# Kernel tuning notes

Measured on AMD Instinct MI355X. Metric: run time of the kernel, lower is better.

Reference implementation:

```python
import jax, jax.numpy as jnp
import numpy as np

NOISE_EPS = 1e-2   # Shazeer noisy-gating stddev floor
LN_EPS = 1e-6
LOSS_COEF = 0.01
K = 2              # num_activated_experts


def _layer_norm(x, w, b):
    mu = jnp.mean(x, axis=-1, keepdims=True)
    var = jnp.var(x, axis=-1, keepdims=True)
    return (x - mu) * jax.lax.rsqrt(var + LN_EPS) * w + b


def _cv_squared(v):
    return jnp.var(v) / (jnp.mean(v) ** 2 + 1e-10)


def _normal_cdf(z):
    return 0.5 * (1.0 + jax.scipy.special.erf(z / jnp.sqrt(jnp.asarray(2.0, z.dtype))))


def setup_inputs() -> dict:
    key = jax.random.key(0)
    ks = jax.random.split(key, 8)
    N, D, H, O, E = 8192, 512, 1024, 512, 8
    x = jax.random.normal(ks[0], (N, D), jnp.float32)
    x_offsets = jnp.sort(jax.random.randint(ks[1], (17,), 0, N)).astype(jnp.int64)
    noise = jax.random.normal(ks[2], (N, E), jnp.float32)
    s = 0.02
    return {
        "x": x,
        "x_offsets": x_offsets,
        "max_seq_len": 2048,
        "noise": noise,
        "norm_w": jnp.ones((D,), jnp.float32),
        "norm_bias": jnp.zeros((D,), jnp.float32),
        "w_gate": jax.random.normal(ks[3], (D, E), jnp.float32) * s,
        "w_noise": jax.random.normal(ks[4], (D, E), jnp.float32) * s,
        "W1": jax.random.normal(ks[5], (E, H, D), jnp.float32) * s,  # [E, model_d, input]
        "b1": jnp.zeros((E, H), jnp.float32),
        "W2": jax.random.normal(ks[6], (E, O, H), jnp.float32) * s,  # [E, output, model_d]
        "b2": jnp.zeros((E, O), jnp.float32),
        "output_weight": jax.random.normal(ks[7], (D, O), jnp.float32) * s,
    }


def reference(x, x_offsets, max_seq_len, noise, norm_w, norm_bias, w_gate, w_noise,
              W1, b1, W2, b2, output_weight):
    N, D = x.shape
    E = w_gate.shape[1]
    k_plus = min(K + 1, E)

    # pre-norm
    x_norm = _layer_norm(x, norm_w, norm_bias)

    # noisy top-k gating (training path)
    clean_logits = x_norm @ w_gate                      # [N, E]
    noise_stddev = jax.nn.softplus(x_norm @ w_noise) + NOISE_EPS
    noisy_logits = clean_logits + noise * noise_stddev

    top_logits, top_indices = jax.lax.top_k(noisy_logits, k_plus)   # [N, k+1]
    top_k_logits = top_logits[:, :K]
    top_k_indices = top_indices[:, :K]
    top_k_gates = jax.nn.softmax(top_k_logits, axis=-1)             # [N, K]

    rows = jnp.arange(N)[:, None]
    gates = jnp.zeros((N, E), top_k_gates.dtype).at[rows, top_k_indices].set(top_k_gates)

    # load = prob each expert is in top-k under the gating noise (Shazeer)
    flat = top_logits.reshape(-1)
    pos_in = jnp.arange(N) * k_plus + K
    thr_in = flat[pos_in][:, None]          # (k+1)-th value: threshold if already in
    thr_out = flat[pos_in - 1][:, None]     # k-th value: threshold if currently out
    is_in = noisy_logits > thr_in
    prob_in = _normal_cdf((clean_logits - thr_in) / noise_stddev)
    prob_out = _normal_cdf((clean_logits - thr_out) / noise_stddev)
    load_probs = jnp.where(is_in, prob_in, prob_out)                # [N, E]

    loss = LOSS_COEF * (_cv_squared(gates.sum(0)) + _cv_squared(load_probs.sum(0)))

    # dispatch stats: tokens per expert
    lengths = jnp.zeros((E,), jnp.float32).at[top_k_indices.reshape(-1)].add(1.0)
    load = lengths / lengths.sum()

    # grouped expert MLP (dense one-hot combine; gates are 0 for unrouted experts)
    h = jnp.einsum('nd,ehd->neh', x_norm, W1) + b1                  # [N, E, H]
    a = jax.nn.silu(h)
    y_e = jnp.einsum('neh,eoh->neo', a, W2) + b2                    # [N, E, O]
    y_moe = jnp.einsum('ne,neo->no', gates, y_e)                    # [N, O]

    # shared expert: addmm(y, shared_x=x, output_weight)
    y = y_moe + x @ output_weight
    return y, loss, load
```

## Files before the change

kernel.cpp:

```cpp
#include <hip/hip_runtime.h>
#include <math.h>

typedef unsigned short u16;
typedef unsigned int u32;

#define N_ROWS 8192
#define DDIM 512
#define HDIM 1024
#define ODIM 512
#define NEXP 8
#define MAXPAIRS (N_ROWS * 2)
#define MAXPOS (MAXPAIRS + NEXP * 128)
#define MAXTILES (MAXPOS / 128)

#define SM_CNT 0
#define SM_CUR 8
#define SM_AOFF 16
#define SM_GSUM 32
#define SM_LSUM 40
#define SM_WORDS 64

using short8 = __attribute__((ext_vector_type(8))) short;
using float4v = __attribute__((ext_vector_type(4))) float;

__device__ __forceinline__ u16 f2bf(float f) {
    union { float f; u32 u; } v; v.f = f;
    u32 u = v.u;
    return (u16)((u + 0x7fffu + ((u >> 16) & 1u)) >> 16);
}

__device__ __forceinline__ void async_copy16(u16* lds, const u16* g) {
    __builtin_amdgcn_global_load_lds(
        (const __attribute__((address_space(1))) void*)g,
        (__attribute__((address_space(3))) void*)lds, 16, 0, 0);
}

__global__ __launch_bounds__(256) void init_kernel(int* small, int* bucket_rows, float* zeropage) {
    int i = blockIdx.x * 256 + threadIdx.x;
    if (i < SM_WORDS) small[i] = 0;
    if (i < 512) zeropage[i] = 0.f;
    if (i < MAXPOS) bucket_rows[i] = -1;
}

__global__ __launch_bounds__(256) void convert_w_kernel(const float* __restrict__ W1, const float* __restrict__ W2,
                                                        u16* __restrict__ W1b, u16* __restrict__ W2b) {
    const size_t n4 = (size_t)NEXP * HDIM * DDIM / 4;
    size_t i = (size_t)blockIdx.x * 256 + threadIdx.x;
    const float* src; u16* dst;
    if (i < n4) { src = W1; dst = W1b; } else { src = W2; dst = W2b; i -= n4; }
    float4 v = ((const float4*)src)[i];
    ushort4 o;
    o.x = f2bf(v.x); o.y = f2bf(v.y); o.z = f2bf(v.z); o.w = f2bf(v.w);
    ((ushort4*)dst)[i] = o;
}

__global__ __launch_bounds__(256) void transpose_ow_kernel(const float* __restrict__ ow, u16* __restrict__ owT) {
    __shared__ float tile[32][33];
    int bx = blockIdx.x * 32, by = blockIdx.y * 32;
    int tx = threadIdx.x & 31, ty = threadIdx.x >> 5;
    for (int r = ty; r < 32; r += 8) tile[r][tx] = ow[(size_t)(by + r) * ODIM + bx + tx];
    __syncthreads();
    for (int r = ty; r < 32; r += 8) owT[(size_t)(bx + r) * DDIM + by + tx] = f2bf(tile[tx][r]);
}

__global__ __launch_bounds__(256) void gating_kernel(
    const float* __restrict__ x, const float* __restrict__ noise,
    const float* __restrict__ norm_w, const float* __restrict__ norm_b,
    const float* __restrict__ w_gate, const float* __restrict__ w_noise,
    u16* __restrict__ xnorm_bf, u16* __restrict__ x_bf,
    int* __restrict__ pair_expert, float* __restrict__ pair_gate,
    int* __restrict__ small)
{
    __shared__ float wgT[NEXP * DDIM];
    __shared__ float wnT[NEXP * DDIM];
    __shared__ float blk_g[NEXP];
    __shared__ float blk_l[NEXP];
    __shared__ int blk_c[NEXP];
    float* smf = (float*)small;

    int tid = threadIdx.x;
    for (int i = tid; i < NEXP * DDIM; i += 256) {
        int d = i >> 3, e = i & 7;
        wgT[e * DDIM + d] = w_gate[i];
        wnT[e * DDIM + d] = w_noise[i];
    }
    if (tid < NEXP) { blk_g[tid] = 0.f; blk_l[tid] = 0.f; blk_c[tid] = 0; }
    __syncthreads();

    int wave = tid >> 6, lane = tid & 63;
    float nw[8], nb[8];
#pragma unroll
    for (int j = 0; j < 8; j++) { nw[j] = norm_w[j * 64 + lane]; nb[j] = norm_b[j * 64 + lane]; }

    for (int r = 0; r < 4; ++r) {
        int row = blockIdx.x * 16 + wave * 4 + r;
        const float* xr = x + (size_t)row * DDIM;
        float xv[8], s = 0.f, s2 = 0.f;
#pragma unroll
        for (int j = 0; j < 8; j++) { float v = xr[j * 64 + lane]; xv[j] = v; s += v; s2 += v * v; }
#pragma unroll
        for (int o = 32; o; o >>= 1) { s += __shfl_xor(s, o, 64); s2 += __shfl_xor(s2, o, 64); }
        float mu = s * (1.f / DDIM);
        float var = s2 * (1.f / DDIM) - mu * mu;
        float rstd = rsqrtf(var + 1e-6f);

        float acc[16];
#pragma unroll
        for (int e = 0; e < 16; e++) acc[e] = 0.f;
#pragma unroll
        for (int j = 0; j < 8; j++) {
            float v = (xv[j] - mu) * rstd * nw[j] + nb[j];
            int d = j * 64 + lane;
            xnorm_bf[(size_t)row * DDIM + d] = f2bf(v);
            x_bf[(size_t)row * DDIM + d] = f2bf(xv[j]);
#pragma unroll
            for (int e = 0; e < 8; e++) {
                acc[e] += v * wgT[e * DDIM + d];
                acc[8 + e] += v * wnT[e * DDIM + d];
            }
        }
#pragma unroll
        for (int e = 0; e < 16; e++)
#pragma unroll
            for (int o = 32; o; o >>= 1) acc[e] += __shfl_xor(acc[e], o, 64);

        float cl[8], sd[8], nz[8];
#pragma unroll
        for (int e = 0; e < 8; e++) {
            cl[e] = acc[e];
            float t = acc[8 + e];
            float sp = fmaxf(t, 0.f) + log1pf(expf(-fabsf(t)));
            sd[e] = sp + 0.01f;
            nz[e] = cl[e] + noise[(size_t)row * NEXP + e] * sd[e];
        }
        int idx[3]; float val[3]; u32 msk = 0;
#pragma unroll
        for (int t = 0; t < 3; t++) {
            float best = -INFINITY; int bi = 0;
#pragma unroll
            for (int e = 0; e < 8; e++)
                if (!((msk >> e) & 1) && nz[e] > best) { best = nz[e]; bi = e; }
            idx[t] = bi; val[t] = best; msk |= 1u << bi;
        }
        float e1 = expf(val[1] - val[0]);
        float g0 = 1.f / (1.f + e1), g1 = e1 / (1.f + e1);
        float thr_in = val[2], thr_out = val[1];

        if (lane == 0) {
            pair_expert[row * 2] = idx[0]; pair_gate[row * 2] = g0;
            pair_expert[row * 2 + 1] = idx[1]; pair_gate[row * 2 + 1] = g1;
            atomicAdd(&blk_g[idx[0]], g0); atomicAdd(&blk_g[idx[1]], g1);
            atomicAdd(&blk_c[idx[0]], 1); atomicAdd(&blk_c[idx[1]], 1);
#pragma unroll
            for (int e = 0; e < 8; e++) {
                float thr = (nz[e] > thr_in) ? thr_in : thr_out;
                float z = (cl[e] - thr) / sd[e];
                float p = 0.5f * (1.f + erff(z * 0.70710678118654752f));
                atomicAdd(&blk_l[e], p);
            }
        }
    }
    __syncthreads();
    if (tid < NEXP) {
        atomicAdd(smf + SM_GSUM + tid, blk_g[tid]);
        atomicAdd(smf + SM_LSUM + tid, blk_l[tid]);
        atomicAdd(&small[SM_CNT + tid], blk_c[tid]);
    }
}

__global__ void prefix_kernel(int* small) {
    if (threadIdx.x == 0 && blockIdx.x == 0) {
        int acc = 0;
        small[SM_AOFF] = 0;
        for (int e = 0; e < NEXP; e++) {
            acc += (small[SM_CNT + e] + 127) & ~127;
            small[SM_AOFF + e + 1] = acc;
        }
    }
}

__global__ __launch_bounds__(256) void scatter_kernel(const int* __restrict__ pair_expert, int* small,
                                                      int* __restrict__ bucket_rows, int* __restrict__ pair_pos) {
    __shared__ int blk_cnt[NEXP];
    __shared__ int blk_base[NEXP];
    int tid = threadIdx.x;
    if (tid < NEXP) blk_cnt[tid] = 0;
    __syncthreads();
    int p = blockIdx.x * 256 + tid;
    int e = pair_expert[p];
    int local = atomicAdd(&blk_cnt[e], 1);
    __syncthreads();
    if (tid < NEXP)
        blk_base[tid] = small[SM_AOFF + tid] + atomicAdd(&small[SM_CUR + tid], blk_cnt[tid]);
    __syncthreads();
    int pos = blk_base[e] + local;
    bucket_rows[pos] = p >> 1;
    pair_pos[p] = pos;
}

template <int MODE>
__global__ __launch_bounds__(256) void gemm_kernel(
    const u16* __restrict__ A, const u16* __restrict__ Bw,
    const int* __restrict__ bucket_rows, const int* __restrict__ small,
    const float* __restrict__ bias, const u16* __restrict__ zeropage,
    u16* __restrict__ out_bf, float* __restrict__ out_f)
{
    constexpr int KD = (MODE == 1) ? 1024 : 512;
    constexpr int ND = (MODE == 0) ? 1024 : 512;
    __shared__ __align__(16) u16 As[128 * 32];
    __shared__ __align__(16) u16 Bs[128 * 32];

    int tid = threadIdx.x;
    int e = 0;
    int base = blockIdx.x * 128;
    if constexpr (MODE == 0 || MODE == 1) {
        if (base >= small[SM_AOFF + 8]) return;
        while (e < 7 && base >= small[SM_AOFF + e + 1]) ++e;
    }

    int wave = tid >> 6, lane = tid & 63;
    const int trow = wave * 32 + (lane >> 2);
    const int kcol = (lane & 3) * 8;
    const u16 *ga0, *ga1;
    if constexpr (MODE == 0) {
        int r0 = bucket_rows[base + trow];
        int r1 = bucket_rows[base + trow + 16];
        ga0 = ((r0 < 0) ? zeropage : A + (size_t)r0 * KD) + kcol;
        ga1 = ((r1 < 0) ? zeropage : A + (size_t)r1 * KD) + kcol;
    } else {
        ga0 = A + (size_t)(base + trow) * KD + kcol;
        ga1 = A + (size_t)(base + trow + 16) * KD + kcol;
    }
    const u16* Bsel = Bw + ((MODE == 2) ? 0 : (size_t)e * ND * KD);
    int bn = blockIdx.y * 128;
    const u16* gb0 = Bsel + (size_t)(bn + trow) * KD + kcol;
    const u16* gb1 = Bsel + (size_t)(bn + trow + 16) * KD + kcol;
    u16* lA0 = &As[(wave * 32) * 32];
    u16* lA1 = &As[(wave * 32 + 16) * 32];
    u16* lB0 = &Bs[(wave * 32) * 32];
    u16* lB1 = &Bs[(wave * 32 + 16) * 32];

    int wm = (wave & 1) * 64, wn = (wave >> 1) * 64;
    int fr = lane & 15, kg = (lane >> 4) * 8;

    float4v acc[4][4];
#pragma unroll
    for (int i = 0; i < 4; i++)
#pragma unroll
        for (int j = 0; j < 4; j++) acc[i][j] = (float4v){0.f, 0.f, 0.f, 0.f};

    for (int k0 = 0; k0 < KD; k0 += 32) {
        __syncthreads();
        async_copy16(lA0, ga0 + k0);
        async_copy16(lA1, ga1 + k0);
        async_copy16(lB0, gb0 + k0);
        async_copy16(lB1, gb1 + k0);
        __syncthreads();
        short8 af[4], bf[4];
#pragma unroll
        for (int mt = 0; mt < 4; mt++) af[mt] = *(const short8*)&As[(wm + mt * 16 + fr) * 32 + kg];
#pragma unroll
        for (int nt = 0; nt < 4; nt++) bf[nt] = *(const short8*)&Bs[(wn + nt * 16 + fr) * 32 + kg];
#pragma unroll
        for (int mt = 0; mt < 4; mt++)
#pragma unroll
            for (int nt = 0; nt < 4; nt++)
                acc[mt][nt] = __builtin_amdgcn_mfma_f32_16x16x32_bf16(af[mt], bf[nt], acc[mt][nt], 0, 0, 0);
    }

    int rbase = (lane >> 4) * 4, c16 = lane & 15;
#pragma unroll
    for (int nt = 0; nt < 4; nt++) {
        int gn = bn + wn + nt * 16 + c16;
        float bv = 0.f;
        if constexpr (MODE == 0) bv = bias[e * ND + gn];
#pragma unroll
        for (int mt = 0; mt < 4; mt++) {
            int gm = base + wm + mt * 16 + rbase;
#pragma unroll
            for (int r = 0; r < 4; r++) {
                float v = acc[mt][nt][r];
                if constexpr (MODE == 0) {
                    float h = v + bv;
                    float a = h * __builtin_amdgcn_rcpf(1.f + __expf(-h));
                    out_bf[(size_t)(gm + r) * ND + gn] = f2bf(a);
                } else {
                    out_f[(size_t)(gm + r) * ND + gn] = v;
                }
            }
        }
    }
}

__global__ __launch_bounds__(128) void combine_kernel(
    float* __restrict__ y, const float* __restrict__ ypair,
    const int* __restrict__ pair_expert, const float* __restrict__ pair_gate,
    const int* __restrict__ pair_pos, const float* __restrict__ b2)
{
    int row = blockIdx.x;
    int e0 = pair_expert[row * 2], e1 = pair_expert[row * 2 + 1];
    float g0 = pair_gate[row * 2], g1 = pair_gate[row * 2 + 1];
    int p0 = pair_pos[row * 2], p1 = pair_pos[row * 2 + 1];
    int i = threadIdx.x;
    const float4* a0 = (const float4*)(ypair + (size_t)p0 * ODIM);
    const float4* a1 = (const float4*)(ypair + (size_t)p1 * ODIM);
    const float4* c0 = (const float4*)(b2 + (size_t)e0 * ODIM);
    const float4* c1 = (const float4*)(b2 + (size_t)e1 * ODIM);
    float4* yr = (float4*)(y + (size_t)row * ODIM);
    float4 v = yr[i], u0 = a0[i], u1 = a1[i], w0 = c0[i], w1 = c1[i];
    v.x += g0 * (u0.x + w0.x) + g1 * (u1.x + w1.x);
    v.y += g0 * (u0.y + w0.y) + g1 * (u1.y + w1.y);
    v.z += g0 * (u0.z + w0.z) + g1 * (u1.z + w1.z);
    v.w += g0 * (u0.w + w0.w) + g1 * (u1.w + w1.w);
    yr[i] = v;
}

__global__ void loss_kernel(const int* __restrict__ small, float* __restrict__ out_loss, float* __restrict__ out_load) {
    if (threadIdx.x == 0 && blockIdx.x == 0) {
        const float* gs = (const float*)small + SM_GSUM;
        const float* ls = (const float*)small + SM_LSUM;
        float cv[2];
        for (int t = 0; t < 2; t++) {
            const float* v = t ? ls : gs;
            float m = 0.f;
            for (int e = 0; e < NEXP; e++) m += v[e];
            m *= (1.f / NEXP);
            float var = 0.f;
            for (int e = 0; e < NEXP; e++) { float d = v[e] - m; var += d * d; }
            var *= (1.f / NEXP);
            cv[t] = var / (m * m + 1e-10f);
        }
        out_loss[0] = 0.01f * (cv[0] + cv[1]);
        int tot = 0;
        for (int e = 0; e < NEXP; e++) tot += small[SM_CNT + e];
        float inv = 1.f / (float)tot;
        for (int e = 0; e < NEXP; e++) out_load[e] = (float)small[SM_CNT + e] * inv;
    }
}

extern "C" void kernel_launch(void* const* d_in, const int* in_sizes, int n_in,
                              void* d_out, int out_size, void* d_ws, size_t ws_size,
                              hipStream_t stream)
{
    (void)in_sizes; (void)n_in; (void)out_size; (void)ws_size;
    const float* x = (const float*)d_in[0];
    const float* noise = (const float*)d_in[3];
    const float* norm_w = (const float*)d_in[4];
    const float* norm_b = (const float*)d_in[5];
    const float* w_gate = (const float*)d_in[6];
    const float* w_noise = (const float*)d_in[7];
    const float* W1 = (const float*)d_in[8];
    const float* b1 = (const float*)d_in[9];
    const float* W2 = (const float*)d_in[10];
    const float* b2 = (const float*)d_in[11];
    const float* ow = (const float*)d_in[12];

    float* y = (float*)d_out;
    float* out_loss = y + (size_t)N_ROWS * ODIM;
    float* out_load = out_loss + 1;

    char* ws = (char*)d_ws;
    size_t off = 0;
    auto alloc = [&](size_t b) { size_t p = off; off = (off + b + 255) & ~(size_t)255; return p; };
    u16* xnorm_bf = (u16*)(ws + alloc((size_t)N_ROWS * DDIM * 2));
    u16* x_bf     = (u16*)(ws + alloc((size_t)N_ROWS * DDIM * 2));
    u16* W1b      = (u16*)(ws + alloc((size_t)NEXP * HDIM * DDIM * 2));
    u16* W2b      = (u16*)(ws + alloc((size_t)NEXP * ODIM * HDIM * 2));
    u16* owT      = (u16*)(ws + alloc((size_t)DDIM * ODIM * 2));
    u16* a_buf    = (u16*)(ws + alloc((size_t)MAXPOS * HDIM * 2));
    float* ypair  = (float*)(ws + alloc((size_t)MAXPOS * ODIM * 4));
    int* pair_expert = (int*)(ws + alloc((size_t)MAXPAIRS * 4));
    float* pair_gate = (float*)(ws + alloc((size_t)MAXPAIRS * 4));
    int* pair_pos    = (int*)(ws + alloc((size_t)MAXPAIRS * 4));
    int* bucket_rows = (int*)(ws + alloc((size_t)MAXPOS * 4));
    int* small       = (int*)(ws + alloc(SM_WORDS * 4));
    float* zeropage  = (float*)(ws + alloc(2048));

    init_kernel<<<MAXPOS / 256, 256, 0, stream>>>(small, bucket_rows, zeropage);
    convert_w_kernel<<<8192, 256, 0, stream>>>(W1, W2, W1b, W2b);
    transpose_ow_kernel<<<dim3(16, 16), 256, 0, stream>>>(ow, owT);
    gating_kernel<<<N_ROWS / 16, 256, 0, stream>>>(x, noise, norm_w, norm_b, w_gate, w_noise,
                                                   xnorm_bf, x_bf, pair_expert, pair_gate, small);
    prefix_kernel<<<1, 1, 0, stream>>>(small);
    scatter_kernel<<<MAXPAIRS / 256, 256, 0, stream>>>(pair_expert, small, bucket_rows, pair_pos);
    gemm_kernel<0><<<dim3(MAXTILES, HDIM / 128), 256, 0, stream>>>(xnorm_bf, W1b, bucket_rows, small,
                                                                   b1, (const u16*)zeropage, a_buf, nullptr);
    gemm_kernel<1><<<dim3(MAXTILES, ODIM / 128), 256, 0, stream>>>(a_buf, W2b, bucket_rows, small,
                                                                   nullptr, (const u16*)zeropage, nullptr, ypair);
    gemm_kernel<2><<<dim3(N_ROWS / 128, ODIM / 128), 256, 0, stream>>>(x_bf, owT, bucket_rows, small,
                                                                       nullptr, (const u16*)zeropage, nullptr, y);
    combine_kernel<<<N_ROWS, 128, 0, stream>>>(y, ypair, pair_expert, pair_gate, pair_pos, b2);
    loss_kernel<<<1, 64, 0, stream>>>(small, out_loss, out_load);
}
```

Baseline: 275.6 us.

## Fuse MoE pipeline launches and scatter-add expert outputs directly into y

Merges init, weight conversion and transpose into one prep kernel. Folds the prefix sum and loss computation into the scatter kernel. Runs the shared-expert GEMM in the same launch as the first expert GEMM. Replaces the ypair buffer and the combine kernel with gated atomic adds from the second GEMM epilogue, which removes several launches and a large fp32 intermediate round-trip. In exchange it adds atomic contention on y and makes the summation order nondeterministic.

```diff
diff --git a/kernel.cpp b/kernel.cpp
--- a/kernel.cpp
+++ b/kernel.cpp
@@ -35,32 +35,36 @@
         (__attribute__((address_space(3))) void*)lds, 16, 0, 0);
 }
 
-__global__ __launch_bounds__(256) void init_kernel(int* small, int* bucket_rows, float* zeropage) {
-    int i = blockIdx.x * 256 + threadIdx.x;
-    if (i < SM_WORDS) small[i] = 0;
-    if (i < 512) zeropage[i] = 0.f;
-    if (i < MAXPOS) bucket_rows[i] = -1;
-}
-
-__global__ __launch_bounds__(256) void convert_w_kernel(const float* __restrict__ W1, const float* __restrict__ W2,
-                                                        u16* __restrict__ W1b, u16* __restrict__ W2b) {
-    const size_t n4 = (size_t)NEXP * HDIM * DDIM / 4;
-    size_t i = (size_t)blockIdx.x * 256 + threadIdx.x;
-    const float* src; u16* dst;
-    if (i < n4) { src = W1; dst = W1b; } else { src = W2; dst = W2b; i -= n4; }
-    float4 v = ((const float4*)src)[i];
-    ushort4 o;
-    o.x = f2bf(v.x); o.y = f2bf(v.y); o.z = f2bf(v.z); o.w = f2bf(v.w);
-    ((ushort4*)dst)[i] = o;
-}
-
-__global__ __launch_bounds__(256) void transpose_ow_kernel(const float* __restrict__ ow, u16* __restrict__ owT) {
+#define CONV_BLOCKS 8192
+__global__ __launch_bounds__(256) void prep_kernel(
+    const float* __restrict__ W1, const float* __restrict__ W2, const float* __restrict__ ow,
+    u16* __restrict__ W1b, u16* __restrict__ W2b, u16* __restrict__ owT,
+    int* __restrict__ small, int* __restrict__ bucket_rows, float* __restrict__ zeropage)
+{
     __shared__ float tile[32][33];
-    int bx = blockIdx.x * 32, by = blockIdx.y * 32;
-    int tx = threadIdx.x & 31, ty = threadIdx.x >> 5;
-    for (int r = ty; r < 32; r += 8) tile[r][tx] = ow[(size_t)(by + r) * ODIM + bx + tx];
-    __syncthreads();
-    for (int r = ty; r < 32; r += 8) owT[(size_t)(bx + r) * DDIM + by + tx] = f2bf(tile[tx][r]);
+    int b = blockIdx.x, tid = threadIdx.x;
+    if (b < CONV_BLOCKS) {
+        const size_t n4 = (size_t)NEXP * HDIM * DDIM / 4;
+        size_t i = (size_t)b * 256 + tid;
+        const float* src; u16* dst;
+        if (i < n4) { src = W1; dst = W1b; } else { src = W2; dst = W2b; i -= n4; }
+        float4 v = ((const float4*)src)[i];
+        ushort4 o;
+        o.x = f2bf(v.x); o.y = f2bf(v.y); o.z = f2bf(v.z); o.w = f2bf(v.w);
+        ((ushort4*)dst)[i] = o;
+    } else if (b < CONV_BLOCKS + 256) {
+        int t = b - CONV_BLOCKS;
+        int bx = (t & 15) * 32, by = (t >> 4) * 32;
+        int tx = tid & 31, ty = tid >> 5;
+        for (int r = ty; r < 32; r += 8) tile[r][tx] = ow[(size_t)(by + r) * ODIM + bx + tx];
+        __syncthreads();
+        for (int r = ty; r < 32; r += 8) owT[(size_t)(bx + r) * DDIM + by + tx] = f2bf(tile[tx][r]);
+    } else {
+        int i = (b - CONV_BLOCKS - 256) * 256 + tid;
+        if (i < SM_WORDS) small[i] = 0;
+        if (i < 512) zeropage[i] = 0.f;
+        if (i < MAXPOS) bucket_rows[i] = -1;
+    }
 }
 
 __global__ __launch_bounds__(256) void gating_kernel(
@@ -168,22 +172,19 @@
     }
 }
 
-__global__ void prefix_kernel(int* small) {
-    if (threadIdx.x == 0 && blockIdx.x == 0) {
-        int acc = 0;
-        small[SM_AOFF] = 0;
-        for (int e = 0; e < NEXP; e++) {
-            acc += (small[SM_CNT + e] + 127) & ~127;
-            small[SM_AOFF + e + 1] = acc;
-        }
-    }
-}
-
-__global__ __launch_bounds__(256) void scatter_kernel(const int* __restrict__ pair_expert, int* small,
-                                                      int* __restrict__ bucket_rows, int* __restrict__ pair_pos) {
+__global__ __launch_bounds__(256) void scatter_kernel(
+    const int* __restrict__ pair_expert, const float* __restrict__ pair_gate,
+    int* __restrict__ small, int* __restrict__ bucket_rows, float* __restrict__ gate_by_pos,
+    float* __restrict__ out_loss, float* __restrict__ out_load)
+{
+    __shared__ int aoff[NEXP + 1];
     __shared__ int blk_cnt[NEXP];
     __shared__ int blk_base[NEXP];
     int tid = threadIdx.x;
+    if (tid == 0) {
+        int acc = 0; aoff[0] = 0;
+        for (int e = 0; e < NEXP; e++) { acc += (small[SM_CNT + e] + 127) & ~127; aoff[e + 1] = acc; }
+    }
     if (tid < NEXP) blk_cnt[tid] = 0;
     __syncthreads();
     int p = blockIdx.x * 256 + tid;
@@ -191,48 +192,77 @@
     int local = atomicAdd(&blk_cnt[e], 1);
     __syncthreads();
     if (tid < NEXP)
-        blk_base[tid] = small[SM_AOFF + tid] + atomicAdd(&small[SM_CUR + tid], blk_cnt[tid]);
+        blk_base[tid] = aoff[tid] + atomicAdd(&small[SM_CUR + tid], blk_cnt[tid]);
+    if (blockIdx.x == 0 && tid < NEXP + 1) small[SM_AOFF + tid] = aoff[tid];
     __syncthreads();
     int pos = blk_base[e] + local;
     bucket_rows[pos] = p >> 1;
-    pair_pos[p] = pos;
-}
-
-template <int MODE>
-__global__ __launch_bounds__(256) void gemm_kernel(
-    const u16* __restrict__ A, const u16* __restrict__ Bw,
+    gate_by_pos[pos] = pair_gate[p];
+
+    if (blockIdx.x == 0 && tid == 0) {
+        const float* gs = (const float*)small + SM_GSUM;
+        const float* ls = (const float*)small + SM_LSUM;
+        float cv[2];
+        for (int t = 0; t < 2; t++) {
+            const float* v = t ? ls : gs;
+            float m = 0.f;
+            for (int k = 0; k < NEXP; k++) m += v[k];
+            m *= (1.f / NEXP);
+            float var = 0.f;
+            for (int k = 0; k < NEXP; k++) { float d = v[k] - m; var += d * d; }
+            var *= (1.f / NEXP);
+            cv[t] = var / (m * m + 1e-10f);
+        }
+        out_loss[0] = 0.01f * (cv[0] + cv[1]);
+        int tot = 0;
+        for (int k = 0; k < NEXP; k++) tot += small[SM_CNT + k];
+        float inv = 1.f / (float)tot;
+        for (int k = 0; k < NEXP; k++) out_load[k] = (float)small[SM_CNT + k] * inv;
+    }
+}
+
+__global__ __launch_bounds__(256) void gemmA_kernel(
+    const u16* __restrict__ xnorm, const u16* __restrict__ xbf,
+    const u16* __restrict__ W1b, const u16* __restrict__ owT,
     const int* __restrict__ bucket_rows, const int* __restrict__ small,
-    const float* __restrict__ bias, const u16* __restrict__ zeropage,
-    u16* __restrict__ out_bf, float* __restrict__ out_f)
-{
-    constexpr int KD = (MODE == 1) ? 1024 : 512;
-    constexpr int ND = (MODE == 0) ? 1024 : 512;
+    const float* __restrict__ b1, const u16* __restrict__ zeropage,
+    u16* __restrict__ a_buf, float* __restrict__ y)
+{
+    constexpr int KD = 512;
     __shared__ __align__(16) u16 As[128 * 32];
     __shared__ __align__(16) u16 Bs[128 * 32];
 
     int tid = threadIdx.x;
-    int e = 0;
-    int base = blockIdx.x * 128;
-    if constexpr (MODE == 0 || MODE == 1) {
+    bool m0 = blockIdx.y < 8;
+    int base, bn, e = 0;
+    const u16* Bsel;
+    if (m0) {
+        base = blockIdx.x * 128;
         if (base >= small[SM_AOFF + 8]) return;
         while (e < 7 && base >= small[SM_AOFF + e + 1]) ++e;
+        bn = blockIdx.y * 128;
+        Bsel = W1b + (size_t)e * HDIM * KD;
+    } else {
+        int j = (blockIdx.y - 8) * 136 + blockIdx.x;
+        if (j >= 256) return;
+        base = (j >> 2) * 128;
+        bn = (j & 3) * 128;
+        Bsel = owT;
     }
 
     int wave = tid >> 6, lane = tid & 63;
     const int trow = wave * 32 + (lane >> 2);
     const int kcol = (lane & 3) * 8;
     const u16 *ga0, *ga1;
-    if constexpr (MODE == 0) {
+    if (m0) {
         int r0 = bucket_rows[base + trow];
         int r1 = bucket_rows[base + trow + 16];
-        ga0 = ((r0 < 0) ? zeropage : A + (size_t)r0 * KD) + kcol;
-        ga1 = ((r1 < 0) ? zeropage : A + (size_t)r1 * KD) + kcol;
+        ga0 = ((r0 < 0) ? zeropage : xnorm + (size_t)r0 * KD) + kcol;
+        ga1 = ((r1 < 0) ? zeropage : xnorm + (size_t)r1 * KD) + kcol;
     } else {
-        ga0 = A + (size_t)(base + trow) * KD + kcol;
-        ga1 = A + (size_t)(base + trow + 16) * KD + kcol;
-    }
-    const u16* Bsel = Bw + ((MODE == 2) ? 0 : (size_t)e * ND * KD);
-    int bn = blockIdx.y * 128;
+        ga0 = xbf + (size_t)(base + trow) * KD + kcol;
+        ga1 = xbf + (size_t)(base + trow + 16) * KD + kcol;
+    }
     const u16* gb0 = Bsel + (size_t)(bn + trow) * KD + kcol;
     const u16* gb1 = Bsel + (size_t)(bn + trow + 16) * KD + kcol;
     u16* lA0 = &As[(wave * 32) * 32];
@@ -272,69 +302,100 @@
 #pragma unroll
     for (int nt = 0; nt < 4; nt++) {
         int gn = bn + wn + nt * 16 + c16;
-        float bv = 0.f;
-        if constexpr (MODE == 0) bv = bias[e * ND + gn];
+        float bv = m0 ? b1[e * HDIM + gn] : 0.f;
 #pragma unroll
         for (int mt = 0; mt < 4; mt++) {
             int gm = base + wm + mt * 16 + rbase;
 #pragma unroll
             for (int r = 0; r < 4; r++) {
                 float v = acc[mt][nt][r];
-                if constexpr (MODE == 0) {
+                if (m0) {
                     float h = v + bv;
                     float a = h * __builtin_amdgcn_rcpf(1.f + __expf(-h));
-                    out_bf[(size_t)(gm + r) * ND + gn] = f2bf(a);
+                    a_buf[(size_t)(gm + r) * HDIM + gn] = f2bf(a);
                 } else {
-                    out_f[(size_t)(gm + r) * ND + gn] = v;
+                    y[(size_t)(gm + r) * ODIM + gn] = v;
                 }
             }
         }
     }
 }
 
-__global__ __launch_bounds__(128) void combine_kernel(
-    float* __restrict__ y, const float* __restrict__ ypair,
-    const int* __restrict__ pair_expert, const float* __restrict__ pair_gate,
-    const int* __restrict__ pair_pos, const float* __restrict__ b2)
-{
-    int row = blockIdx.x;
-    int e0 = pair_expert[row * 2], e1 = pair_expert[row * 2 + 1];
-    float g0 = pair_gate[row * 2], g1 = pair_gate[row * 2 + 1];
-    int p0 = pair_pos[row * 2], p1 = pair_pos[row * 2 + 1];
-    int i = threadIdx.x;
-    const float4* a0 = (const float4*)(ypair + (size_t)p0 * ODIM);
-    const float4* a1 = (const float4*)(ypair + (size_t)p1 * ODIM);
-    const float4* c0 = (const float4*)(b2 + (size_t)e0 * ODIM);
-    const float4* c1 = (const float4*)(b2 + (size_t)e1 * ODIM);
-    float4* yr = (float4*)(y + (size_t)row * ODIM);
-    float4 v = yr[i], u0 = a0[i], u1 = a1[i], w0 = c0[i], w1 = c1[i];
-    v.x += g0 * (u0.x + w0.x) + g1 * (u1.x + w1.x);
-    v.y += g0 * (u0.y + w0.y) + g1 * (u1.y + w1.y);
-    v.z += g0 * (u0.z + w0.z) + g1 * (u1.z + w1.z);
-    v.w += g0 * (u0.w + w0.w) + g1 * (u1.w + w1.w);
-    yr[i] = v;
-}
-
-__global__ void loss_kernel(const int* __restrict__ small, float* __restrict__ out_loss, float* __restrict__ out_load) {
-    if (threadIdx.x == 0 && blockIdx.x == 0) {
-        const float* gs = (const float*)small + SM_GSUM;
-        const float* ls = (const float*)small + SM_LSUM;
-        float cv[2];
-        for (int t = 0; t < 2; t++) {
-            const float* v = t ? ls : gs;
-            float m = 0.f;
-            for (int e = 0; e < NEXP; e++) m += v[e];
-            m *= (1.f / NEXP);
-            float var = 0.f;
-            for (int e = 0; e < NEXP; e++) { float d = v[e] - m; var += d * d; }
-            var *= (1.f / NEXP);
-            cv[t] = var / (m * m + 1e-10f);
-        }
-        out_loss[0] = 0.01f * (cv[0] + cv[1]);
-        int tot = 0;
-        for (int e = 0; e < NEXP; e++) tot += small[SM_CNT + e];
-        float inv = 1.f / (float)tot;
-        for (int e = 0; e < NEXP; e++) out_load[e] = (float)small[SM_CNT + e] * inv;
+__global__ __launch_bounds__(256) void gemmB_kernel(
+    const u16* __restrict__ a_buf, const u16* __restrict__ W2b,
+    const int* __restrict__ bucket_rows, const int* __restrict__ small,
+    const float* __restrict__ b2, const float* __restrict__ gate_by_pos,
+    float* __restrict__ y)
+{
+    constexpr int KD = 1024;
+    __shared__ __align__(16) u16 As[128 * 32];
+    __shared__ __align__(16) u16 Bs[128 * 32];
+
+    int tid = threadIdx.x;
+    int base = blockIdx.x * 128;
+    if (base >= small[SM_AOFF + 8]) return;
+    int e = 0;
+    while (e < 7 && base >= small[SM_AOFF + e + 1]) ++e;
+    int bn = blockIdx.y * 128;
+
+    int wave = tid >> 6, lane = tid & 63;
+    const int trow = wave * 32 + (lane >> 2);
+    const int kcol = (lane & 3) * 8;
+    const u16* ga0 = a_buf + (size_t)(base + trow) * KD + kcol;
+    const u16* ga1 = a_buf + (size_t)(base + trow + 16) * KD + kcol;
+    const u16* Bsel = W2b + (size_t)e * ODIM * KD;
+    const u16* gb0 = Bsel + (size_t)(bn + trow) * KD + kcol;
+    const u16* gb1 = Bsel + (size_t)(bn + trow + 16) * KD + kcol;
+    u16* lA0 = &As[(wave * 32) * 32];
+    u16* lA1 = &As[(wave * 32 + 16) * 32];
+    u16* lB0 = &Bs[(wave * 32) * 32];
+    u16* lB1 = &Bs[(wave * 32 + 16) * 32];
+
+    int wm = (wave & 1) * 64, wn = (wave >> 1) * 64;
+    int fr = lane & 15, kg = (lane >> 4) * 8;
+
+    float4v acc[4][4];
+#pragma unroll
+    for (int i = 0; i < 4; i++)
+#pragma unroll
+        for (int j = 0; j < 4; j++) acc[i][j] = (float4v){0.f, 0.f, 0.f, 0.f};
+
+    for (int k0 = 0; k0 < KD; k0 += 32) {
+        __syncthreads();
+        async_copy16(lA0, ga0 + k0);
+        async_copy16(lA1, ga1 + k0);
+        async_copy16(lB0, gb0 + k0);
+        async_copy16(lB1, gb1 + k0);
+        __syncthreads();
+        short8 af[4], bf[4];
+#pragma unroll
+        for (int mt = 0; mt < 4; mt++) af[mt] = *(const short8*)&As[(wm + mt * 16 + fr) * 32 + kg];
+#pragma unroll
+        for (int nt = 0; nt < 4; nt++) bf[nt] = *(const short8*)&Bs[(wn + nt * 16 + fr) * 32 + kg];
+#pragma unroll
+        for (int mt = 0; mt < 4; mt++)
+#pragma unroll
+            for (int nt = 0; nt < 4; nt++)
+                acc[mt][nt] = __builtin_amdgcn_mfma_f32_16x16x32_bf16(af[mt], bf[nt], acc[mt][nt], 0, 0, 0);
+    }
+
+    int rbase = (lane >> 4) * 4, c16 = lane & 15;
+#pragma unroll
+    for (int mt = 0; mt < 4; mt++) {
+        int pos0 = base + wm + mt * 16 + rbase;
+        int rows[4]; float gs[4];
+#pragma unroll
+        for (int r = 0; r < 4; r++) { rows[r] = bucket_rows[pos0 + r]; gs[r] = gate_by_pos[pos0 + r]; }
+#pragma unroll
+        for (int nt = 0; nt < 4; nt++) {
+            int gn = bn + wn + nt * 16 + c16;
+            float b2v = b2[e * ODIM + gn];
+#pragma unroll
+            for (int r = 0; r < 4; r++) {
+                if (rows[r] >= 0)
+                    unsafeAtomicAdd(&y[(size_t)rows[r] * ODIM + gn], gs[r] * (acc[mt][nt][r] + b2v));
+            }
+        }
     }
 }
 
@@ -368,27 +429,21 @@
     u16* W2b      = (u16*)(ws + alloc((size_t)NEXP * ODIM * HDIM * 2));
     u16* owT      = (u16*)(ws + alloc((size_t)DDIM * ODIM * 2));
     u16* a_buf    = (u16*)(ws + alloc((size_t)MAXPOS * HDIM * 2));
-    float* ypair  = (float*)(ws + alloc((size_t)MAXPOS * ODIM * 4));
     int* pair_expert = (int*)(ws + alloc((size_t)MAXPAIRS * 4));
     float* pair_gate = (float*)(ws + alloc((size_t)MAXPAIRS * 4));
-    int* pair_pos    = (int*)(ws + alloc((size_t)MAXPAIRS * 4));
+    float* gate_by_pos = (float*)(ws + alloc((size_t)MAXPOS * 4));
     int* bucket_rows = (int*)(ws + alloc((size_t)MAXPOS * 4));
     int* small       = (int*)(ws + alloc(SM_WORDS * 4));
     float* zeropage  = (float*)(ws + alloc(2048));
 
-    init_kernel<<<MAXPOS / 256, 256, 0, stream>>>(small, bucket_rows, zeropage);
-    convert_w_kernel<<<8192, 256, 0, stream>>>(W1, W2, W1b, W2b);
-    transpose_ow_kernel<<<dim3(16, 16), 256, 0, stream>>>(ow, owT);
+    prep_kernel<<<CONV_BLOCKS + 256 + 68, 256, 0, stream>>>(W1, W2, ow, W1b, W2b, owT,
+                                                            small, bucket_rows, zeropage);
     gating_kernel<<<N_ROWS / 16, 256, 0, stream>>>(x, noise, norm_w, norm_b, w_gate, w_noise,
                                                    xnorm_bf, x_bf, pair_expert, pair_gate, small);
-    prefix_kernel<<<1, 1, 0, stream>>>(small);
-    scatter_kernel<<<MAXPAIRS / 256, 256, 0, stream>>>(pair_expert, small, bucket_rows, pair_pos);
-    gemm_kernel<0><<<dim3(MAXTILES, HDIM / 128), 256, 0, stream>>>(xnorm_bf, W1b, bucket_rows, small,
-                                                                   b1, (const u16*)zeropage, a_buf, nullptr);
-    gemm_kernel<1><<<dim3(MAXTILES, ODIM / 128), 256, 0, stream>>>(a_buf, W2b, bucket_rows, small,
-                                                                   nullptr, (const u16*)zeropage, nullptr, ypair);
-    gemm_kernel<2><<<dim3(N_ROWS / 128, ODIM / 128), 256, 0, stream>>>(x_bf, owT, bucket_rows, small,
-                                                                       nullptr, (const u16*)zeropage, nullptr, y);
-    combine_kernel<<<N_ROWS, 128, 0, stream>>>(y, ypair, pair_expert, pair_gate, pair_pos, b2);
-    loss_kernel<<<1, 64, 0, stream>>>(small, out_loss, out_load);
-}
+    scatter_kernel<<<MAXPAIRS / 256, 256, 0, stream>>>(pair_expert, pair_gate, small,
+                                                       bucket_rows, gate_by_pos, out_loss, out_load);
+    gemmA_kernel<<<dim3(MAXTILES, 10), 256, 0, stream>>>(xnorm_bf, x_bf, W1b, owT, bucket_rows,
+                                                         small, b1, (const u16*)zeropage, a_buf, y);
+    gemmB_kernel<<<dim3(MAXTILES, ODIM / 128), 256, 0, stream>>>(a_buf, W2b, bucket_rows, small,
+                                                                 b2, gate_by_pos, y);
+}
```

Result: no change. 278.3 us (+1.0%).
